# Optimization experiments

Hardware: AMD Instinct MI355X
Metric: run time of the kernel (lower is better)

The kernel has to match this reference:

```python
import jax, jax.numpy as jnp
import numpy as np

SELF_ATTN = -5e4  # reformer TOKEN_SELF_ATTN_VALUE


def _lsh_self_attention(h, w_qk, w_v, w_out, b_out, rotations, n_heads, bucket_size):
    # h: [B, N, D] with N divisible by 2*bucket_size (pre-padded)
    B, N, D = h.shape
    E = D // n_heads
    n_buckets = N // bucket_size
    n_hashes = rotations.shape[1]
    # shared-QK projections, heads merged into batch (batch-major, like reformer)
    qk = (h @ w_qk).reshape(B, N, n_heads, E).transpose(0, 2, 1, 3).reshape(B * n_heads, N, E)
    v = (h @ w_v).reshape(B, N, n_heads, E).transpose(0, 2, 1, 3).reshape(B * n_heads, N, E)
    # --- LSH hashing: argmax over [rot, -rot] ---
    rot = jnp.einsum('bne,ehr->bhnr', qk, rotations)          # [BH, n_hashes, N, n_buckets/2]
    rot = jnp.concatenate([rot, -rot], axis=-1)               # [BH, n_hashes, N, n_buckets]
    buckets = jnp.argmax(rot, axis=-1)                        # [BH, n_hashes, N]
    buckets = buckets + (jnp.arange(n_hashes) * n_buckets)[None, :, None]
    buckets = buckets.reshape(B * n_heads, n_hashes * N)
    # --- sort tokens by (bucket, position) ---
    ticker = jnp.arange(n_hashes * N)
    buckets_and_t = N * buckets + (ticker % N)                # unique keys -> deterministic sort
    sticker = jnp.argsort(buckets_and_t, axis=-1)
    undo = jnp.argsort(sticker, axis=-1)
    st = sticker % N                                          # original positions, sorted order
    sqk = jnp.take_along_axis(qk, st[..., None], axis=1)      # [BH, n_hashes*N, E]
    sv = jnp.take_along_axis(v, st[..., None], axis=1)
    # --- chunk and attend locally (with look-one-back) ---
    nc = n_hashes * n_buckets
    bq = sqk.reshape(-1, nc, bucket_size, E)
    bk = bq / jnp.maximum(jnp.linalg.norm(bq, axis=-1, keepdims=True), 1e-12)  # normalized shared keys
    bv = sv.reshape(-1, nc, bucket_size, E)
    bts = st.reshape(-1, nc, bucket_size)
    look = lambda t: jnp.concatenate([t, jnp.roll(t, 1, axis=1)], axis=2)
    bk, bv, bkt = look(bk), look(bv), look(bts)
    dots = jnp.einsum('bcie,bcje->bcij', bq, bk) * (E ** -0.5)  # [BH, nc, bs, 2*bs]
    dots = jnp.where(bts[..., :, None] == bkt[..., None, :], SELF_ATTN, dots)  # mask self
    lse = jax.scipy.special.logsumexp(dots, axis=-1, keepdims=True)
    p = jnp.exp(dots - lse)
    bo = jnp.einsum('bcij,bcje->bcie', p, bv)
    so = bo.reshape(-1, n_hashes * N, E)
    slog = lse.reshape(-1, n_hashes * N)
    # --- unsort and combine hash rounds by softmax over logsumexp logits ---
    o = jnp.take_along_axis(so, undo[..., None], axis=1).reshape(-1, n_hashes, N, E)
    logits = jnp.take_along_axis(slog, undo, axis=1).reshape(-1, n_hashes, N, 1)
    probs = jnp.exp(logits - jax.scipy.special.logsumexp(logits, axis=1, keepdims=True))
    out = jnp.sum(o * probs, axis=1)                          # [BH, N, E]
    out = out.reshape(B, n_heads, N, E).transpose(0, 2, 1, 3).reshape(B, N, D)
    return out @ w_out + b_out


def setup_inputs() -> dict:
    key = jax.random.key(0)
    ks = jax.random.split(key, 8)
    b, l, n = 16, 12, 325
    d_feat, d_pos, heads, bucket, n_hashes = 256, 64, 8, 16, 4
    pad = 2 * bucket - n % (2 * bucket)
    n_buckets = (n + pad) // bucket
    E = d_feat // heads
    s = 0.05
    return {
        'x': jax.random.normal(ks[0], (b, l, n, d_feat), dtype=jnp.float32),
        'ste': jax.random.normal(ks[1], (b, l, n, d_pos), dtype=jnp.float32),
        'w_proj': jax.random.normal(ks[2], (d_feat + d_pos, d_feat), dtype=jnp.float32) * s,
        'b_proj': jnp.zeros((d_feat,), jnp.float32),
        'w_qk': jax.random.normal(ks[3], (d_feat, d_feat), dtype=jnp.float32) * s,
        'w_v': jax.random.normal(ks[4], (d_feat, d_feat), dtype=jnp.float32) * s,
        'w_out': jax.random.normal(ks[5], (d_feat, d_feat), dtype=jnp.float32) * s,
        'b_out': jnp.zeros((d_feat,), jnp.float32),
        'rotations': jax.random.normal(ks[6], (E, n_hashes, n_buckets // 2), dtype=jnp.float32),
        'n_heads': heads,
        'bucket_size': bucket,
    }


def reference(x, ste, w_proj, b_proj, w_qk, w_v, w_out, b_out, rotations, n_heads, bucket_size):
    b, l, n, d = x.shape
    h = jnp.concatenate([x, ste], axis=-1).reshape(b * l, n, -1)
    h = h @ w_proj + b_proj                                   # projection to d_hidden_feat
    pad = 2 * bucket_size - n % (2 * bucket_size)             # always > 0 (as in the source)
    h = jnp.pad(h, ((0, 0), (0, pad), (0, 0)))
    h = _lsh_self_attention(h, w_qk, w_v, w_out, b_out, rotations, n_heads, bucket_size)
    h = h[:, :-pad, :]
    return h.reshape(b, l, n, -1)
```

## Files before the change

### kernel.cpp

```cpp
#include <hip/hip_runtime.h>
#include <math.h>

#define BL 192
#define NREAL 325
#define NPAD 352
#define DM 256
#define DPOS 64
#define DIN 320
#define NHEADS 8
#define EDIM 32
#define NHASH 4
#define BS 16
#define NBUCK 22
#define NCHUNK 88
#define BHTOT 1536
#define RROT 11
#define W2COLS 352
#define RTM 8
#define HTM 16
#define QKP 9
#define CITER 11

__global__ __launch_bounds__(256) void h_kernel(
    const float* __restrict__ x, const float* __restrict__ ste,
    const float* __restrict__ wproj, const float* __restrict__ bproj,
    float* __restrict__ h) {
  int tile = blockIdx.x, bl = blockIdx.y;
  int d = threadIdx.x;
  int n0 = tile * HTM;
  float acc[HTM];
#pragma unroll
  for (int m = 0; m < HTM; ++m) acc[m] = 0.f;
  if (n0 + HTM <= NREAL) {
    const float* xb = x + (size_t)(bl * NREAL + n0) * DM;
    const float* sb = ste + (size_t)(bl * NREAL + n0) * DPOS;
    for (int k = 0; k < DM; k += 4) {
      float b0 = wproj[(k + 0) * DM + d];
      float b1 = wproj[(k + 1) * DM + d];
      float b2 = wproj[(k + 2) * DM + d];
      float b3 = wproj[(k + 3) * DM + d];
#pragma unroll
      for (int m = 0; m < HTM; ++m) {
        const float* xr = xb + (size_t)m * DM + k;
        acc[m] = fmaf(xr[0], b0, acc[m]);
        acc[m] = fmaf(xr[1], b1, acc[m]);
        acc[m] = fmaf(xr[2], b2, acc[m]);
        acc[m] = fmaf(xr[3], b3, acc[m]);
      }
    }
    for (int k = 0; k < DPOS; k += 4) {
      float b0 = wproj[(DM + k + 0) * DM + d];
      float b1 = wproj[(DM + k + 1) * DM + d];
      float b2 = wproj[(DM + k + 2) * DM + d];
      float b3 = wproj[(DM + k + 3) * DM + d];
#pragma unroll
      for (int m = 0; m < HTM; ++m) {
        const float* sr = sb + (size_t)m * DPOS + k;
        acc[m] = fmaf(sr[0], b0, acc[m]);
        acc[m] = fmaf(sr[1], b1, acc[m]);
        acc[m] = fmaf(sr[2], b2, acc[m]);
        acc[m] = fmaf(sr[3], b3, acc[m]);
      }
    }
  } else if (n0 < NREAL) {
#pragma unroll
    for (int m = 0; m < HTM; ++m) {
      if (n0 + m < NREAL) {
        const float* xr = x + (size_t)(bl * NREAL + n0 + m) * DM;
        const float* sr = ste + (size_t)(bl * NREAL + n0 + m) * DPOS;
        for (int k = 0; k < DM; ++k) acc[m] = fmaf(xr[k], wproj[k * DM + d], acc[m]);
        for (int k = 0; k < DPOS; ++k)
          acc[m] = fmaf(sr[k], wproj[(DM + k) * DM + d], acc[m]);
      }
    }
  }
  float bb = bproj[d];
#pragma unroll
  for (int m = 0; m < HTM; ++m) {
    int n = n0 + m;
    h[((size_t)(bl * NPAD + n)) * DM + d] = (n < NREAL) ? (acc[m] + bb) : 0.f;
  }
}

__global__ __launch_bounds__(256) void qkv_rot_bucket_kernel(
    const float* __restrict__ h, const float* __restrict__ wqk,
    const float* __restrict__ wv, const float* __restrict__ rotations,
    int* __restrict__ buckets, float* __restrict__ qk_out,
    float* __restrict__ v_out) {
  int tile = blockIdx.x, bl = blockIdx.y;
  int tid = threadIdx.x;
  __shared__ float Qs[RTM][DM];
  __shared__ float Rs[RTM][W2COLS];
  int n0 = tile * RTM;
  const float* hb = h + (size_t)(bl * NPAD + n0) * DM;
  float aq[RTM], av[RTM];
#pragma unroll
  for (int m = 0; m < RTM; ++m) { aq[m] = 0.f; av[m] = 0.f; }
  for (int k = 0; k < DM; k += 4) {
    float q0 = wqk[(k + 0) * DM + tid];
    float q1 = wqk[(k + 1) * DM + tid];
    float q2 = wqk[(k + 2) * DM + tid];
    float q3 = wqk[(k + 3) * DM + tid];
    float w0 = wv[(k + 0) * DM + tid];
    float w1 = wv[(k + 1) * DM + tid];
    float w2 = wv[(k + 2) * DM + tid];
    float w3 = wv[(k + 3) * DM + tid];
#pragma unroll
    for (int m = 0; m < RTM; ++m) {
      const float* hr = hb + (size_t)m * DM + k;
      float a0 = hr[0], a1 = hr[1], a2 = hr[2], a3 = hr[3];
      aq[m] = fmaf(a0, q0, aq[m]);
      aq[m] = fmaf(a1, q1, aq[m]);
      aq[m] = fmaf(a2, q2, aq[m]);
      aq[m] = fmaf(a3, q3, aq[m]);
      av[m] = fmaf(a0, w0, av[m]);
      av[m] = fmaf(a1, w1, av[m]);
      av[m] = fmaf(a2, w2, av[m]);
      av[m] = fmaf(a3, w3, av[m]);
    }
  }
  {
    int head = tid >> 5, e = tid & 31;
    size_t bh = (size_t)(bl * NHEADS + head);
#pragma unroll
    for (int m = 0; m < RTM; ++m) {
      Qs[m][tid] = aq[m];
      int n = n0 + m;
      qk_out[(bh * NPAD + n) * EDIM + e] = aq[m];
      v_out[(bh * NPAD + n) * EDIM + e] = av[m];
    }
  }
  __syncthreads();
  for (int col = tid; col < W2COLS; col += 256) {
    int head = col / 44;
    int hr = col - head * 44;
    int hs = hr / RROT;
    int r = hr - hs * RROT;
    float acc[RTM];
#pragma unroll
    for (int m = 0; m < RTM; ++m) acc[m] = 0.f;
    {
#pragma clang fp contract(off)
      for (int e = 0; e < EDIM; ++e) {
        float rr = rotations[(e * NHASH + hs) * RROT + r];
#pragma unroll
        for (int m = 0; m < RTM; ++m) {
          float p = Qs[m][head * EDIM + e] * rr;
          acc[m] = acc[m] + p;
        }
      }
    }
#pragma unroll
    for (int m = 0; m < RTM; ++m) Rs[m][col] = acc[m];
  }
  __syncthreads();
  {
    int m = tid >> 5;
    int rest = tid & 31;
    int head = rest >> 2;
    int hs = rest & 3;
    int cbase = head * 44 + hs * RROT;
    float bestv = Rs[m][cbase];
    int best = 0;
    for (int r = 1; r < RROT; ++r) {
      float dv = Rs[m][cbase + r];
      if (dv > bestv) { bestv = dv; best = r; }
    }
    for (int r = 0; r < RROT; ++r) {
      float dv = -Rs[m][cbase + r];
      if (dv > bestv) { bestv = dv; best = RROT + r; }
    }
    int n = n0 + m;
    int bh = bl * NHEADS + head;
    buckets[((size_t)(bh * NHASH + hs)) * NPAD + n] = best;
  }
}

__global__ __launch_bounds__(384) void sort_kernel(const int* __restrict__ buckets,
                                                   int* __restrict__ st) {
  int bh = blockIdx.x, hs = blockIdx.y;
  int n = threadIdx.x;
  __shared__ int buck[NPAD];
  const int* brow = buckets + ((size_t)(bh * NHASH + hs)) * NPAD;
  if (n < NPAD) buck[n] = brow[n];
  __syncthreads();
  if (n < NPAD) {
    int b = buck[n];
    int dest = 0;
    for (int m2 = 0; m2 < NPAD; ++m2) {
      int bm = buck[m2];
      dest += (int)((bm < b) | ((bm == b) & (m2 < n)));
    }
    st[((size_t)(bh * NHASH + hs)) * NPAD + dest] = n;
  }
}

__global__ __launch_bounds__(512) void attn_fused_kernel(
    const float* __restrict__ qk, const float* __restrict__ v,
    const int* __restrict__ st, float* __restrict__ att) {
  int bh = blockIdx.x;
  int t = threadIdx.x;
  int w = t >> 6;
  int lane = t & 63;
  int i2 = lane >> 5;
  int j = lane & 31;

  __shared__ float4 qk4[NPAD][QKP];
  __shared__ int stf[NHASH * NPAD];
  __shared__ float ll_s[NHASH][NPAD];
  __shared__ float rnorm_s[NPAD];
  __shared__ float L_s[NPAD];
  __shared__ float psw_all[8][16 * 36];

  const float* qk_s = (const float*)qk4;
  const float* qkb = qk + (size_t)bh * NPAD * EDIM;
  const float* vb = v + (size_t)bh * NPAD * EDIM;
  const int* strow = st + (size_t)bh * (NHASH * NPAD);

  float dsave[CITER][8];

  for (int idx = t; idx < NPAD * 8; idx += 512) {
    int n = idx >> 3, c4 = idx & 7;
    qk4[n][c4] = ((const float4*)qkb)[idx];
  }
  for (int idx = t; idx < NHASH * NPAD; idx += 512) stf[idx] = strow[idx];
  __syncthreads();
  for (int n = t; n < NPAD; n += 512) {
    const float* row = (const float*)qk4[n];
    float s = 0.f;
    for (int e = 0; e < EDIM; ++e) s = fmaf(row[e], row[e], s);
    rnorm_s[n] = 1.0f / fmaxf(sqrtf(s), 1e-12f);
  }
  __syncthreads();

#pragma unroll
  for (int ci = 0; ci < CITER; ++ci) {
    int c = w + ci * 8;
    int pc = (c + NCHUNK - 1) % NCHUNK;
    int hs = c / NBUCK;
    int kp = (j < BS) ? stf[c * BS + j] : stf[pc * BS + (j - BS)];
    float kr[EDIM];
    {
      const float4* krow = qk4[kp];
#pragma unroll
      for (int e4 = 0; e4 < 8; ++e4) {
        float4 kv = krow[e4];
        kr[e4 * 4 + 0] = kv.x; kr[e4 * 4 + 1] = kv.y;
        kr[e4 * 4 + 2] = kv.z; kr[e4 * 4 + 3] = kv.w;
      }
    }
    float scale = rnorm_s[kp] * 0.17677669529663688f;
#pragma unroll
    for (int i = 0; i < 8; ++i) {
      int q = i * 2 + i2;
      int qp = stf[c * BS + q];
      const float4* qrow = qk4[qp];
      float dot = 0.f;
#pragma unroll
      for (int e4 = 0; e4 < 8; ++e4) {
        float4 qv = qrow[e4];
        dot = fmaf(qv.x, kr[e4 * 4 + 0], dot);
        dot = fmaf(qv.y, kr[e4 * 4 + 1], dot);
        dot = fmaf(qv.z, kr[e4 * 4 + 2], dot);
        dot = fmaf(qv.w, kr[e4 * 4 + 3], dot);
      }
      dot *= scale;
      if (qp == kp) dot = -50000.0f;
      dsave[ci][i] = dot;
      float mx = dot;
#pragma unroll
      for (int off = 16; off > 0; off >>= 1) mx = fmaxf(mx, __shfl_xor(mx, off, 32));
      float ex = expf(dot - mx);
      float sm = ex;
#pragma unroll
      for (int off = 16; off > 0; off >>= 1) sm += __shfl_xor(sm, off, 32);
      if (j == 0) ll_s[hs][qp] = mx + logf(sm);
    }
  }
  __syncthreads();
  for (int n = t; n < NPAD; n += 512) {
    float l0 = ll_s[0][n], l1 = ll_s[1][n], l2 = ll_s[2][n], l3 = ll_s[3][n];
    float m = fmaxf(fmaxf(l0, l1), fmaxf(l2, l3));
    float s = expf(l0 - m) + expf(l1 - m) + expf(l2 - m) + expf(l3 - m);
    L_s[n] = m + logf(s);
  }
  __syncthreads();

  int head = bh & 7, bl = bh >> 3;
  float* attb = att + ((size_t)bl * NPAD) * DM + head * EDIM;
  float* psw = psw_all[w];
#pragma unroll
  for (int ci = 0; ci < CITER; ++ci) {
    int c = w + ci * 8;
    int pc = (c + NCHUNK - 1) % NCHUNK;
    float vr[32];
#pragma unroll
    for (int jj = 0; jj < 32; ++jj) {
      int kpj = (jj < BS) ? stf[c * BS + jj] : stf[pc * BS + (jj - BS)];
      vr[jj] = vb[kpj * EDIM + j];
    }
#pragma unroll
    for (int i = 0; i < 8; ++i) {
      int q = i * 2 + i2;
      int qp = stf[c * BS + q];
      psw[q * 36 + j] = expf(dsave[ci][i] - L_s[qp]);
    }
#pragma unroll
    for (int i = 0; i < 8; ++i) {
      int q = i * 2 + i2;
      int qp = stf[c * BS + q];
      const float4* prow = (const float4*)(psw + q * 36);
      float acc = 0.f;
#pragma unroll
      for (int j4 = 0; j4 < 8; ++j4) {
        float4 pv = prow[j4];
        acc = fmaf(pv.x, vr[j4 * 4 + 0], acc);
        acc = fmaf(pv.y, vr[j4 * 4 + 1], acc);
        acc = fmaf(pv.z, vr[j4 * 4 + 2], acc);
        acc = fmaf(pv.w, vr[j4 * 4 + 3], acc);
      }
      atomicAdd(&attb[(size_t)qp * DM + j], acc);
    }
  }
}

__global__ __launch_bounds__(256) void outproj_kernel(
    const float* __restrict__ att, const float* __restrict__ w,
    const float* __restrict__ bias, float* __restrict__ out) {
  int tile = blockIdx.x, bl = blockIdx.y;
  int d = threadIdx.x;
  int n0 = tile * HTM;
  float acc[HTM];
#pragma unroll
  for (int m = 0; m < HTM; ++m) acc[m] = 0.f;
  if (n0 + HTM <= NREAL) {
    const float* ab = att + (size_t)(bl * NPAD + n0) * DM;
    for (int k = 0; k < DM; k += 4) {
      float b0 = w[(k + 0) * DM + d];
      float b1 = w[(k + 1) * DM + d];
      float b2 = w[(k + 2) * DM + d];
      float b3 = w[(k + 3) * DM + d];
#pragma unroll
      for (int m = 0; m < HTM; ++m) {
        const float* ar = ab + (size_t)m * DM + k;
        acc[m] = fmaf(ar[0], b0, acc[m]);
        acc[m] = fmaf(ar[1], b1, acc[m]);
        acc[m] = fmaf(ar[2], b2, acc[m]);
        acc[m] = fmaf(ar[3], b3, acc[m]);
      }
    }
  } else if (n0 < NREAL) {
#pragma unroll
    for (int m = 0; m < HTM; ++m) {
      if (n0 + m < NREAL) {
        const float* ar = att + (size_t)(bl * NPAD + n0 + m) * DM;
        for (int k = 0; k < DM; ++k) acc[m] = fmaf(ar[k], w[k * DM + d], acc[m]);
      }
    }
  } else {
    return;
  }
  float bb = bias[d];
#pragma unroll
  for (int m = 0; m < HTM; ++m) {
    int n = n0 + m;
    if (n < NREAL) out[((size_t)(bl * NREAL + n)) * DM + d] = acc[m] + bb;
  }
}

extern "C" void kernel_launch(void* const* d_in, const int* in_sizes, int n_in,
                              void* d_out, int out_size, void* d_ws, size_t ws_size,
                              hipStream_t stream) {
  (void)in_sizes; (void)n_in; (void)out_size;
  const float* x = (const float*)d_in[0];
  const float* ste = (const float*)d_in[1];
  const float* w_proj = (const float*)d_in[2];
  const float* b_proj = (const float*)d_in[3];
  const float* w_qk = (const float*)d_in[4];
  const float* w_v = (const float*)d_in[5];
  const float* w_out = (const float*)d_in[6];
  const float* b_out = (const float*)d_in[7];
  const float* rotations = (const float*)d_in[8];
  float* out = (float*)d_out;

  const size_t szh = (size_t)BL * NPAD * DM;
  const size_t szst = (size_t)BHTOT * NHASH * NPAD;
  const size_t needed = 3 * szh * 4 + 2 * szst * 4;
  if (ws_size < needed) return;

  float* qk = (float*)d_ws;
  float* v = qk + szh;
  float* att = v + szh;
  float* h = att;
  int* st = (int*)(att + szh);
  int* buckets = st + szst;

  h_kernel<<<dim3(NPAD / HTM, BL), dim3(256), 0, stream>>>(
      x, ste, w_proj, b_proj, h);
  qkv_rot_bucket_kernel<<<dim3(NPAD / RTM, BL), dim3(256), 0, stream>>>(
      h, w_qk, w_v, rotations, buckets, qk, v);
  (void)hipMemsetAsync(att, 0, szh * sizeof(float), stream);
  sort_kernel<<<dim3(BHTOT, NHASH), dim3(384), 0, stream>>>(buckets, st);
  attn_fused_kernel<<<dim3(BHTOT), dim3(512), 0, stream>>>(qk, v, st, att);
  outproj_kernel<<<dim3(21, BL), dim3(256), 0, stream>>>(att, w_out, b_out, out);
}
```

Baseline: 1.461 ms.

## Read QK rows from global memory and replace shuffle logsumexp with shared-memory row sums

```diff
diff --git a/kernel.cpp b/kernel.cpp
--- a/kernel.cpp
+++ b/kernel.cpp
@@ -18,7 +18,6 @@
 #define W2COLS 352
 #define RTM 8
 #define HTM 16
-#define QKP 9
 #define CITER 11
 
 __global__ __launch_bounds__(256) void h_kernel(
@@ -205,33 +204,28 @@
   int i2 = lane >> 5;
   int j = lane & 31;
 
-  __shared__ float4 qk4[NPAD][QKP];
   __shared__ int stf[NHASH * NPAD];
   __shared__ float ll_s[NHASH][NPAD];
   __shared__ float rnorm_s[NPAD];
   __shared__ float L_s[NPAD];
   __shared__ float psw_all[8][16 * 36];
 
-  const float* qk_s = (const float*)qk4;
   const float* qkb = qk + (size_t)bh * NPAD * EDIM;
   const float* vb = v + (size_t)bh * NPAD * EDIM;
   const int* strow = st + (size_t)bh * (NHASH * NPAD);
 
   float dsave[CITER][8];
 
-  for (int idx = t; idx < NPAD * 8; idx += 512) {
-    int n = idx >> 3, c4 = idx & 7;
-    qk4[n][c4] = ((const float4*)qkb)[idx];
-  }
   for (int idx = t; idx < NHASH * NPAD; idx += 512) stf[idx] = strow[idx];
-  __syncthreads();
   for (int n = t; n < NPAD; n += 512) {
-    const float* row = (const float*)qk4[n];
+    const float* row = qkb + n * EDIM;
     float s = 0.f;
     for (int e = 0; e < EDIM; ++e) s = fmaf(row[e], row[e], s);
     rnorm_s[n] = 1.0f / fmaxf(sqrtf(s), 1e-12f);
   }
   __syncthreads();
+
+  float* psw = psw_all[w];
 
 #pragma unroll
   for (int ci = 0; ci < CITER; ++ci) {
@@ -241,7 +235,7 @@
     int kp = (j < BS) ? stf[c * BS + j] : stf[pc * BS + (j - BS)];
     float kr[EDIM];
     {
-      const float4* krow = qk4[kp];
+      const float4* krow = (const float4*)(qkb + kp * EDIM);
 #pragma unroll
       for (int e4 = 0; e4 < 8; ++e4) {
         float4 kv = krow[e4];
@@ -254,7 +248,7 @@
     for (int i = 0; i < 8; ++i) {
       int q = i * 2 + i2;
       int qp = stf[c * BS + q];
-      const float4* qrow = qk4[qp];
+      const float4* qrow = (const float4*)(qkb + qp * EDIM);
       float dot = 0.f;
 #pragma unroll
       for (int e4 = 0; e4 < 8; ++e4) {
@@ -267,14 +261,21 @@
       dot *= scale;
       if (qp == kp) dot = -50000.0f;
       dsave[ci][i] = dot;
-      float mx = dot;
-#pragma unroll
-      for (int off = 16; off > 0; off >>= 1) mx = fmaxf(mx, __shfl_xor(mx, off, 32));
-      float ex = expf(dot - mx);
-      float sm = ex;
-#pragma unroll
-      for (int off = 16; off > 0; off >>= 1) sm += __shfl_xor(sm, off, 32);
-      if (j == 0) ll_s[hs][qp] = mx + logf(sm);
+      psw[q * 36 + j] = expf(dot);
+    }
+    {
+      int r = lane & 15;
+      const float4* prow = (const float4*)(psw + r * 36);
+      float sm = 0.f;
+#pragma unroll
+      for (int j4 = 0; j4 < 8; ++j4) {
+        float4 pv = prow[j4];
+        sm = sm + pv.x + pv.y + pv.z + pv.w;
+      }
+      if (lane < 16) {
+        int qp2 = stf[c * BS + lane];
+        ll_s[hs][qp2] = logf(sm);
+      }
     }
   }
   __syncthreads();
@@ -288,7 +289,6 @@
 
   int head = bh & 7, bl = bh >> 3;
   float* attb = att + ((size_t)bl * NPAD) * DM + head * EDIM;
-  float* psw = psw_all[w];
 #pragma unroll
   for (int ci = 0; ci < CITER; ++ci) {
     int c = w + ci * 8;
```

Measured after the change: 1.488 ms. No clear change (+1.8%).
